# Performance work log

Hardware: AMD Instinct MI355X
Metric: run time of the kernel (lower is better)

Reference implementation:

```python
import jax, jax.numpy as jnp
import numpy as np

TEMP = 0.05
MOMENTUM = 0.2
B, D, P = 1024, 2048, 16384


def setup_inputs() -> dict:
    key = jax.random.key(0)
    k1, k2, k3, k4, k5 = jax.random.split(key, 5)
    input_features = jax.random.normal(k1, (B, D), dtype=jnp.float32)
    storage = jax.random.normal(k2, (P, D), dtype=jnp.float32)
    # storage holds L2-normalized proxy centroids
    storage = storage / jnp.linalg.norm(storage, axis=1, keepdims=True)
    camids = jax.random.randint(k3, (B,), 0, 8, dtype=jnp.int64)
    proxy_labels = jax.random.randint(k4, (B,), 0, 2048, dtype=jnp.int64)
    abs_proxy_labels = jax.random.randint(k5, (B,), 0, P, dtype=jnp.int64)
    return {
        "input_features": input_features,
        "storage": storage,
        "camids": camids,
        "proxy_labels": proxy_labels,
        "abs_proxy_labels": abs_proxy_labels,
    }


def reference(input_features, storage, camids, proxy_labels, abs_proxy_labels):
    # logits = x @ storage^T / temp  (dense GEMM vs proxy memory bank)
    logits = jnp.einsum("bd,pd->bp", input_features, storage) / TEMP
    logp = jax.nn.log_softmax(logits, axis=1)
    # NLL loss (mean reduction) over the true absolute proxy index
    loss = -jnp.mean(logp[jnp.arange(logp.shape[0]), abs_proxy_labels])

    # Sequential per-sample momentum-EMA scatter update + row renorm
    # (duplicate indices compound sequentially, matching the torch loop)
    def step(S, xl):
        x, l = xl
        row = MOMENTUM * S[l] + (1.0 - MOMENTUM) * x
        row = row / jnp.linalg.norm(row)
        return S.at[l].set(row), None

    new_storage, _ = jax.lax.scan(step, storage, (input_features, abs_proxy_labels))
    return loss, new_storage
```

## Files before the change

kernel.cpp:

```cpp
#include <hip/hip_runtime.h>
#include <cmath>

constexpr int B_N = 1024;
constexpr int D_N = 2048;
constexpr int P_N = 16384;
constexpr int TILE = 128;
constexpr int BK = 64;
constexpr int NT = P_N / TILE;
constexpr int NIT = D_N / BK;
#define TEMP_INV 20.0f
#define S_SCALE 16.0f
#define LOGIT_SCALE (TEMP_INV / S_SCALE)
#define MOM 0.2f

typedef __attribute__((ext_vector_type(4))) float floatx4;

__device__ __forceinline__ unsigned int pack4_fp8(float4 v) {
    unsigned int w = __builtin_amdgcn_cvt_pk_fp8_f32(v.x, v.y, 0, false);
    w = __builtin_amdgcn_cvt_pk_fp8_f32(v.z, v.w, w, true);
    return w;
}

__device__ __forceinline__ void gl_lds16(const void* g, void* l) {
    __builtin_amdgcn_global_load_lds(
        (const __attribute__((address_space(1))) void*)g,
        (__attribute__((address_space(3))) void*)l, 16, 0, 0);
}

constexpr int S_F4 = P_N * D_N / 4;
constexpr int S_ITER = S_F4 / 1024;
constexpr int X_F4 = B_N * D_N / 4;
constexpr int X_ITER = X_F4 / 1024;
constexpr int TOT_ITER = S_ITER + X_ITER;

__global__ __launch_bounds__(256) void stream_convert_kernel(
    const float* __restrict__ X, const float* __restrict__ S,
    unsigned char* __restrict__ Xf8, unsigned char* __restrict__ Sf8,
    float* __restrict__ out0, float* __restrict__ outS) {
    const int t = threadIdx.x;
    if (blockIdx.x == 0 && t == 0) out0[0] = 0.f;
    for (int bi = blockIdx.x; bi < TOT_ITER; bi += gridDim.x) {
        if (bi < S_ITER) {
            const size_t base = (size_t)bi * 1024;
            const float4* s4 = (const float4*)S + base;
            unsigned int* q = (unsigned int*)Sf8 + base;
            float4 v[4];
#pragma unroll
            for (int j = 0; j < 4; ++j) v[j] = s4[t + j * 256];
            if (outS) {
                float4* o4 = (float4*)outS + base;
#pragma unroll
                for (int j = 0; j < 4; ++j) o4[t + j * 256] = v[j];
            }
#pragma unroll
            for (int j = 0; j < 4; ++j) {
                float4 w = make_float4(v[j].x * S_SCALE, v[j].y * S_SCALE,
                                       v[j].z * S_SCALE, v[j].w * S_SCALE);
                q[t + j * 256] = pack4_fp8(w);
            }
        } else {
            const size_t base = (size_t)(bi - S_ITER) * 1024;
            const float4* x4 = (const float4*)X + base;
            unsigned int* q = (unsigned int*)Xf8 + base;
#pragma unroll
            for (int j = 0; j < 4; ++j) q[t + j * 256] = pack4_fp8(x4[t + j * 256]);
        }
    }
}

__global__ __launch_bounds__(256) void update_kernel(
    const float* __restrict__ X, const float* __restrict__ S,
    const int* __restrict__ labels, float* __restrict__ outS,
    float* __restrict__ ll) {
    __shared__ int sl[B_N];
    __shared__ unsigned long long mask[16];
    __shared__ float red[8];
    __shared__ int s_found;
    const int j = blockIdx.x;
    const int t = threadIdx.x;
    for (int k = t; k < B_N; k += 256) sl[k] = labels[k];
    if (t == 0) s_found = 0;
    if (t < 16) mask[t] = 0ull;
    __syncthreads();
    const int l = sl[j];
    for (int u = 0; u < 4; ++u) {
        int k = u * 256 + t;
        if (k < j && sl[k] == l) s_found = 1;
        if (k > j && sl[k] == l) atomicOr(&mask[k >> 6], 1ull << (k & 63));
    }
    __syncthreads();
    if (s_found) return;

    const float4* s4 = (const float4*)(S + (size_t)l * D_N);
    float4 v0 = s4[t], v1 = s4[256 + t];
    float r[8]  = {v0.x, v0.y, v0.z, v0.w, v1.x, v1.y, v1.z, v1.w};
    float so[8] = {v0.x, v0.y, v0.z, v0.w, v1.x, v1.y, v1.z, v1.w};
    const int lane = t & 63, wv = t >> 6;
    int k = j;
    while (true) {
        const float4* x4 = (const float4*)(X + (size_t)k * D_N);
        float4 a0 = x4[t], a1 = x4[256 + t];
        float xr[8] = {a0.x, a0.y, a0.z, a0.w, a1.x, a1.y, a1.z, a1.w};
        float ss = 0.f, dt = 0.f;
#pragma unroll
        for (int u = 0; u < 8; ++u) {
            r[u] = MOM * r[u] + (1.f - MOM) * xr[u];
            ss += r[u] * r[u];
            dt += so[u] * xr[u];
        }
        for (int off = 32; off; off >>= 1) {
            ss += __shfl_xor(ss, off);
            dt += __shfl_xor(dt, off);
        }
        if (lane == 0) { red[wv] = ss; red[4 + wv] = dt; }
        __syncthreads();
        ss = red[0] + red[1] + red[2] + red[3];
        dt = red[4] + red[5] + red[6] + red[7];
        __syncthreads();
        if (t == 0) ll[k] = dt * TEMP_INV;
        float inv = 1.0f / sqrtf(ss);
#pragma unroll
        for (int u = 0; u < 8; ++u) r[u] *= inv;
        int nk = -1;
        int w0 = k >> 6;
        unsigned long long bb = (mask[w0] >> (k & 63)) >> 1;
        if (bb) nk = k + 1 + (int)__builtin_ctzll(bb);
        else {
            for (int w = w0 + 1; w < 16; ++w) {
                if (mask[w]) { nk = w * 64 + (int)__builtin_ctzll(mask[w]); break; }
            }
        }
        if (nk < 0) break;
        k = nk;
    }
    float4* o4 = (float4*)(outS + (size_t)l * D_N);
    o4[t] = make_float4(r[0], r[1], r[2], r[3]);
    o4[256 + t] = make_float4(r[4], r[5], r[6], r[7]);
}

__device__ __forceinline__ void row_update(
    const float* __restrict__ X, const int* __restrict__ labels,
    int p, int t, float4 v0, float4 v1, float* __restrict__ outS,
    unsigned long long* mask, float* red) {
    if (t < 16) mask[t] = 0ull;
    __syncthreads();
    for (int u = 0; u < 4; ++u) {
        int k = u * 256 + t;
        if (labels[k] == p) atomicOr(&mask[k >> 6], 1ull << (k & 63));
    }
    __syncthreads();
    unsigned long long any = 0;
    for (int w = 0; w < 16; ++w) any |= mask[w];
    float4* o4 = (float4*)(outS + (size_t)p * D_N);
    if (!any) {
        o4[t] = v0; o4[256 + t] = v1;
        return;
    }
    float r[8] = {v0.x, v0.y, v0.z, v0.w, v1.x, v1.y, v1.z, v1.w};
    int k = -1;
    for (int w = 0; w < 16; ++w) {
        if (mask[w]) { k = w * 64 + (int)__builtin_ctzll(mask[w]); break; }
    }
    const int lane = t & 63, wv = t >> 6;
    while (k >= 0) {
        const float4* xk = (const float4*)(X + (size_t)k * D_N);
        float4 a0 = xk[t], a1 = xk[256 + t];
        float xr[8] = {a0.x, a0.y, a0.z, a0.w, a1.x, a1.y, a1.z, a1.w};
        float ss = 0.f;
#pragma unroll
        for (int u = 0; u < 8; ++u) {
            r[u] = MOM * r[u] + (1.f - MOM) * xr[u];
            ss += r[u] * r[u];
        }
        for (int off = 32; off; off >>= 1) ss += __shfl_xor(ss, off);
        if (lane == 0) red[wv] = ss;
        __syncthreads();
        ss = red[0] + red[1] + red[2] + red[3];
        __syncthreads();
        float inv = 1.0f / sqrtf(ss);
#pragma unroll
        for (int u = 0; u < 8; ++u) r[u] *= inv;
        int nk = -1;
        int w0 = k >> 6;
        unsigned long long bb = (mask[w0] >> (k & 63)) >> 1;
        if (bb) nk = k + 1 + (int)__builtin_ctzll(bb);
        else {
            for (int w = w0 + 1; w < 16; ++w) {
                if (mask[w]) { nk = w * 64 + (int)__builtin_ctzll(mask[w]); break; }
            }
        }
        k = nk;
    }
    o4[t] = make_float4(r[0], r[1], r[2], r[3]);
    o4[256 + t] = make_float4(r[4], r[5], r[6], r[7]);
}

__global__ __launch_bounds__(256) void update_copy_kernel(
    const float* __restrict__ X, const float* __restrict__ S,
    const int* __restrict__ labels, float* __restrict__ outS) {
    __shared__ unsigned long long mask[16];
    __shared__ float red[4];
    const int p = blockIdx.x;
    const int t = threadIdx.x;
    const float4* s4 = (const float4*)(S + (size_t)p * D_N);
    float4 v0 = s4[t], v1 = s4[256 + t];
    row_update(X, labels, p, t, v0, v1, outS, mask, red);
}

__global__ __launch_bounds__(256, 4) void gemm_softmax_kernel(
    const unsigned char* __restrict__ Xf8, const unsigned char* __restrict__ Sf8,
    float* __restrict__ part_max, float* __restrict__ part_sum) {
    __shared__ alignas(16) unsigned char sA[2][TILE * BK];
    __shared__ alignas(16) unsigned char sB[2][TILE * BK];
    __shared__ float pmax[2][TILE];
    __shared__ float psum[2][TILE];

    const int t = threadIdx.x;
    const int b = blockIdx.x;
    const int xcd = b & 7;
    const int s = b >> 3;
    const int bm = s >> 4;
    const int bn = (xcd << 4) | (s & 15);
    const int m0 = bm * TILE;
    const int n0 = bn * TILE;

    const int lane = t & 63;
    const int wave = t >> 6;
    const int wm = (wave & 1) * 64;
    const int wn = (wave >> 1) * 64;
    const int frow = lane & 15;
    const int q = lane >> 4;

    const int r0 = t >> 2, r1 = (t + 256) >> 2;
    const int sc0 = ((t & 3) ^ ((r0 & 3) ^ ((r0 >> 2) & 3))) << 4;
    const int sc1 = ((t & 3) ^ ((r1 & 3) ^ ((r1 >> 2) & 3))) << 4;
    const size_t rowA0 = (size_t)(m0 + r0) * D_N + sc0;
    const size_t rowA1 = (size_t)(m0 + r1) * D_N + sc1;
    const size_t rowB0 = (size_t)(n0 + r0) * D_N + sc0;
    const size_t rowB1 = (size_t)(n0 + r1) * D_N + sc1;

#define STAGE(bi, kt) do { const int kof = (kt) * BK;                 \
        gl_lds16(Xf8 + rowA0 + kof, &sA[bi][t * 16]);                 \
        gl_lds16(Xf8 + rowA1 + kof, &sA[bi][(t + 256) * 16]);         \
        gl_lds16(Sf8 + rowB0 + kof, &sB[bi][t * 16]);                 \
        gl_lds16(Sf8 + rowB1 + kof, &sB[bi][(t + 256) * 16]); } while (0)

    const int gswz = (frow & 3) ^ (frow >> 2);
    const int half = (q & 1) * 8;
    const int l0 = q >> 1;
    const int cof0 = (((l0) ^ gswz) << 4) + half;
    const int cof1 = (((l0 | 2) ^ gswz) << 4) + half;
    int aoffs[4], boffs[4];
#pragma unroll
    for (int i = 0; i < 4; ++i) aoffs[i] = (wm + i * 16 + frow) * BK;
#pragma unroll
    for (int j = 0; j < 4; ++j) boffs[j] = (wn + j * 16 + frow) * BK;

    floatx4 acc[4][4];
#pragma unroll
    for (int i = 0; i < 4; ++i)
#pragma unroll
        for (int j = 0; j < 4; ++j)
            acc[i][j] = floatx4{0.f, 0.f, 0.f, 0.f};

    STAGE(0, 0);
    STAGE(1, 1);
    int cur = 0;
    for (int it = 0; it < NIT; ++it) {
        if (it < NIT - 1) asm volatile("s_waitcnt vmcnt(4)" ::: "memory");
        else              asm volatile("s_waitcnt vmcnt(0)" ::: "memory");
        __builtin_amdgcn_s_barrier();
        const unsigned char* pa = &sA[cur][0];
        const unsigned char* pb = &sB[cur][0];
#pragma unroll
        for (int kk = 0; kk < 2; ++kk) {
            const int cof = kk ? cof1 : cof0;
            long long af[4], bf[4];
#pragma unroll
            for (int i = 0; i < 4; ++i)
                af[i] = *(const long long*)(pa + aoffs[i] + cof);
#pragma unroll
            for (int j = 0; j < 4; ++j)
                bf[j] = *(const long long*)(pb + boffs[j] + cof);
#pragma unroll
            for (int i = 0; i < 4; ++i)
#pragma unroll
                for (int j = 0; j < 4; ++j)
                    acc[i][j] = __builtin_amdgcn_mfma_f32_16x16x32_fp8_fp8(
                        af[i], bf[j], acc[i][j], 0, 0, 0);
        }
        __builtin_amdgcn_sched_barrier(0);
        __builtin_amdgcn_s_barrier();
        if (it + 2 < NIT) STAGE(cur, it + 2);
        cur ^= 1;
    }
#undef STAGE

    float lmax[4][4], lsum[4][4];
    for (int i = 0; i < 4; i++) {
        for (int r = 0; r < 4; r++) {
            float m = -INFINITY;
            for (int j = 0; j < 4; j++) m = fmaxf(m, acc[i][j][r] * LOGIT_SCALE);
            for (int off = 1; off < 16; off <<= 1) m = fmaxf(m, __shfl_xor(m, off));
            float s2 = 0.f;
            for (int j = 0; j < 4; j++) s2 += __expf(acc[i][j][r] * LOGIT_SCALE - m);
            for (int off = 1; off < 16; off <<= 1) s2 += __shfl_xor(s2, off);
            lmax[i][r] = m; lsum[i][r] = s2;
        }
    }
    if ((lane & 15) == 0) {
        int lg = lane >> 4;
        for (int i = 0; i < 4; i++)
            for (int r = 0; r < 4; r++) {
                int row = wm + i * 16 + lg * 4 + r;
                pmax[wave >> 1][row] = lmax[i][r];
                psum[wave >> 1][row] = lsum[i][r];
            }
    }
    __syncthreads();
    if (t < TILE) {
        float ma = pmax[0][t], mb = pmax[1][t];
        float M = fmaxf(ma, mb);
        float Sv = psum[0][t] * __expf(ma - M) + psum[1][t] * __expf(mb - M);
        int grow = m0 + t;
        part_max[(size_t)grow * NT + bn] = M;
        part_sum[(size_t)grow * NT + bn] = Sv;
    }
}

__global__ __launch_bounds__(256) void loss_kernel(
    const float* __restrict__ X, const float* __restrict__ S,
    const int* __restrict__ labels,
    const float* __restrict__ part_max, const float* __restrict__ part_sum,
    const float* __restrict__ ll_in, float* __restrict__ out0) {
    const int wave = threadIdx.x >> 6, lane = threadIdx.x & 63;
    const int row = blockIdx.x * 4 + wave;
    float ll;
    if (ll_in) {
        ll = ll_in[row];
    } else {
        const float4* x4 = (const float4*)(X + (size_t)row * D_N);
        const float4* s4 = (const float4*)(S + (size_t)labels[row] * D_N);
        float acc = 0.f;
        for (int k = lane; k < D_N / 4; k += 64) {
            float4 a = x4[k], bb = s4[k];
            acc += a.x * bb.x + a.y * bb.y + a.z * bb.z + a.w * bb.w;
        }
        for (int off = 32; off; off >>= 1) acc += __shfl_xor(acc, off);
        ll = acc * TEMP_INV;
    }
    const float* pm = part_max + (size_t)row * NT;
    const float* ps = part_sum + (size_t)row * NT;
    float m1 = pm[lane], m2 = pm[lane + 64];
    float M = fmaxf(m1, m2);
    for (int off = 32; off; off >>= 1) M = fmaxf(M, __shfl_xor(M, off));
    float Sv = ps[lane] * __expf(m1 - M) + ps[lane + 64] * __expf(m2 - M);
    for (int off = 32; off; off >>= 1) Sv += __shfl_xor(Sv, off);
    float v = ll - (M + __logf(Sv));
    __shared__ float red[4];
    if (lane == 0) red[wave] = v;
    __syncthreads();
    if (threadIdx.x == 0)
        atomicAdd(out0, -(red[0] + red[1] + red[2] + red[3]) * (1.0f / (float)B_N));
}

extern "C" void kernel_launch(void* const* d_in, const int* in_sizes, int n_in,
                              void* d_out, int out_size, void* d_ws, size_t ws_size,
                              hipStream_t stream) {
    const float* X = (const float*)d_in[0];
    const float* S = (const float*)d_in[1];
    const int* labels = (const int*)d_in[4];
    float* out = (float*)d_out;

    const size_t sf8_bytes = (size_t)P_N * D_N;
    const size_t xf8_bytes = (size_t)B_N * D_N;
    const size_t need = sf8_bytes + xf8_bytes + (size_t)B_N * NT * 8
                        + (size_t)B_N * 4 + 64;
    const bool use_ws = (ws_size >= need);

    unsigned char* scratch = use_ws ? (unsigned char*)d_ws
                                    : (unsigned char*)d_out + 16;
    unsigned char* Sf8 = scratch;
    unsigned char* Xf8 = scratch + sf8_bytes;
    float* part_max = (float*)(Xf8 + xf8_bytes);
    float* part_sum = part_max + (size_t)B_N * NT;
    float* ll = part_sum + (size_t)B_N * NT;

    stream_convert_kernel<<<2048, 256, 0, stream>>>(
        X, S, Xf8, Sf8, out, use_ws ? (out + 1) : nullptr);
    if (use_ws)
        update_kernel<<<B_N, 256, 0, stream>>>(X, S, labels, out + 1, ll);
    gemm_softmax_kernel<<<1024, 256, 0, stream>>>(Xf8, Sf8, part_max, part_sum);
    loss_kernel<<<256, 256, 0, stream>>>(X, S, labels, part_max, part_sum,
                                         use_ws ? ll : nullptr, out);
    if (!use_ws)
        update_copy_kernel<<<P_N, 256, 0, stream>>>(X, S, labels, out + 1);
}
```

Baseline: 322.3 us.

## Overlap storage copy to output with FP8 GEMM blocks

Moves the fp32 copy of storage into the output buffer out of the convert kernel and into the GEMM kernel. Each GEMM block copies a 128KB slab using nontemporal loads and stores, even blocks before their compute and odd blocks after it. Because the output is offset by one float, lanes rebuild each misaligned vector with a shuffle. The aim is to hide this memory-bound copy behind compute-bound GEMM work, at the cost of contention inside the GEMM and shuffle overhead. The update kernel now runs after the GEMM so its writes land after the copy.

```diff
diff --git a/kernel.cpp b/kernel.cpp
--- a/kernel.cpp
+++ b/kernel.cpp
@@ -36,7 +36,7 @@
 __global__ __launch_bounds__(256) void stream_convert_kernel(
     const float* __restrict__ X, const float* __restrict__ S,
     unsigned char* __restrict__ Xf8, unsigned char* __restrict__ Sf8,
-    float* __restrict__ out0, float* __restrict__ outS) {
+    float* __restrict__ out0) {
     const int t = threadIdx.x;
     if (blockIdx.x == 0 && t == 0) out0[0] = 0.f;
     for (int bi = blockIdx.x; bi < TOT_ITER; bi += gridDim.x) {
@@ -47,11 +47,6 @@
             float4 v[4];
 #pragma unroll
             for (int j = 0; j < 4; ++j) v[j] = s4[t + j * 256];
-            if (outS) {
-                float4* o4 = (float4*)outS + base;
-#pragma unroll
-                for (int j = 0; j < 4; ++j) o4[t + j * 256] = v[j];
-            }
 #pragma unroll
             for (int j = 0; j < 4; ++j) {
                 float4 w = make_float4(v[j].x * S_SCALE, v[j].y * S_SCALE,
@@ -65,6 +60,30 @@
 #pragma unroll
             for (int j = 0; j < 4; ++j) q[t + j * 256] = pack4_fp8(x4[t + j * 256]);
         }
+    }
+}
+
+__device__ __forceinline__ void copy_block_rows(
+    const float* __restrict__ S, float* __restrict__ outF, int b) {
+    const int t = threadIdx.x;
+    const size_t fbase = (size_t)b * 32768;
+    if (t < 3) {
+        float v = __builtin_nontemporal_load(S + fbase + t);
+        __builtin_nontemporal_store(v, outF + 1 + fbase + t);
+    } else if (t == 3) {
+        float v = __builtin_nontemporal_load(S + fbase + 32767);
+        __builtin_nontemporal_store(v, outF + fbase + 32768);
+    }
+    const floatx4* Sq = (const floatx4*)S + (size_t)b * 8192;
+    floatx4* Oq = (floatx4*)outF + (size_t)b * 8192;
+#pragma unroll 4
+    for (int k = t; k < 8191; k += 256) {
+        floatx4 cur = __builtin_nontemporal_load(Sq + 1 + k);
+        float pw = __shfl_up(cur[3], 1);
+        if ((t & 63) == 0)
+            pw = __builtin_nontemporal_load((const float*)(Sq + 1 + k) - 1);
+        floatx4 o; o[0] = pw; o[1] = cur[0]; o[2] = cur[1]; o[3] = cur[2];
+        __builtin_nontemporal_store(o, Oq + 1 + k);
     }
 }
 
@@ -209,6 +228,7 @@
 
 __global__ __launch_bounds__(256, 4) void gemm_softmax_kernel(
     const unsigned char* __restrict__ Xf8, const unsigned char* __restrict__ Sf8,
+    const float* __restrict__ Sfull, float* __restrict__ outF,
     float* __restrict__ part_max, float* __restrict__ part_sum) {
     __shared__ alignas(16) unsigned char sA[2][TILE * BK];
     __shared__ alignas(16) unsigned char sB[2][TILE * BK];
@@ -217,6 +237,9 @@
 
     const int t = threadIdx.x;
     const int b = blockIdx.x;
+    const bool do_copy = (outF != nullptr);
+    if (do_copy && !(b & 1)) copy_block_rows(Sfull, outF, b);
+
     const int xcd = b & 7;
     const int s = b >> 3;
     const int bm = s >> 4;
@@ -326,6 +349,8 @@
         part_max[(size_t)grow * NT + bn] = M;
         part_sum[(size_t)grow * NT + bn] = Sv;
     }
+
+    if (do_copy && (b & 1)) copy_block_rows(Sfull, outF, b);
 }
 
 __global__ __launch_bounds__(256) void loss_kernel(
@@ -386,11 +411,11 @@
     float* part_sum = part_max + (size_t)B_N * NT;
     float* ll = part_sum + (size_t)B_N * NT;
 
-    stream_convert_kernel<<<2048, 256, 0, stream>>>(
-        X, S, Xf8, Sf8, out, use_ws ? (out + 1) : nullptr);
+    stream_convert_kernel<<<2048, 256, 0, stream>>>(X, S, Xf8, Sf8, out);
+    gemm_softmax_kernel<<<1024, 256, 0, stream>>>(
+        Xf8, Sf8, S, use_ws ? out : nullptr, part_max, part_sum);
     if (use_ws)
         update_kernel<<<B_N, 256, 0, stream>>>(X, S, labels, out + 1, ll);
-    gemm_softmax_kernel<<<1024, 256, 0, stream>>>(Xf8, Sf8, part_max, part_sum);
     loss_kernel<<<256, 256, 0, stream>>>(X, S, labels, part_max, part_sum,
                                          use_ws ? ll : nullptr, out);
     if (!use_ws)
```

Result: slower. 336.7 us (+4.4%).
